# Kernel optimization log

Hardware: AMD Instinct MI355X
Metric: run time of the kernel (lower is better)

Reference implementation:

```python
import jax, jax.numpy as jnp
import numpy as np

B, S, D, E = 4, 2048, 512, 32

def setup_inputs() -> dict:
    key = jax.random.key(0)
    k1, k2, k3 = jax.random.split(key, 3)
    x = jax.random.normal(k1, (B, S, D), dtype=jnp.float32)
    # glorot-ish scaling for weights
    gate_w = jax.random.normal(k2, (D, E), dtype=jnp.float32) * (1.0 / np.sqrt(D))
    gate_b = jnp.zeros((E,), dtype=jnp.float32)
    expert_w = jax.random.normal(k3, (E, D, D), dtype=jnp.float32) * (1.0 / np.sqrt(D))
    return {"x": x, "gate_w": gate_w, "gate_b": gate_b, "expert_w": expert_w}

def reference(x, gate_w, gate_b, expert_w):
    # gate_scores: [B,S,E] (context=None -> route on x itself)
    gate = jax.nn.softmax(jnp.einsum('bsd,de->bse', x, gate_w) + gate_b, axis=-1)
    # Dense soft-MoE: sum_e gate[b,s,e] * (x[b,s,:] @ expert_w[e])
    # Single einsum avoids materializing the [B,S,E,D] intermediate.
    out = jnp.einsum('bse,bsd,edf->bsf', gate, x, expert_w)
    return out
```

## Files before the change

kernel.cpp:

```cpp
#include <hip/hip_runtime.h>

#define TOK 8192
#define DIM 512
#define NE  32
#define KTOT (NE * DIM)

#define BM 128
#define BN 128
#define BK 64

typedef float f32x4 __attribute__((ext_vector_type(4)));
typedef short s16x8 __attribute__((ext_vector_type(8)));

typedef const void __attribute__((address_space(1)))* gp1_t;
typedef void __attribute__((address_space(3)))* lp3_t;

__device__ __forceinline__ void gl_lds16(const void* g, void* l) {
    __builtin_amdgcn_global_load_lds((gp1_t)g, (lp3_t)l, 16, 0, 0);
}

__device__ __forceinline__ ushort f2bf(float f) {
    unsigned u = __builtin_bit_cast(unsigned, f);
    unsigned r = (u + 0x7fffu + ((u >> 16) & 1u)) >> 16;
    return (ushort)r;
}

__global__ __launch_bounds__(256) void k_cvt_wt(const float* __restrict__ w,
                                                ushort* __restrict__ wt) {
    __shared__ float tile[32][33];
    const int e = blockIdx.z;
    const int f0 = blockIdx.x * 32;
    const int d0 = blockIdx.y * 32;
    const int tx = threadIdx.x, ty = threadIdx.y;
    const float* we = w + (size_t)e * DIM * DIM;
#pragma unroll
    for (int i = ty; i < 32; i += 8)
        tile[i][tx] = we[(size_t)(d0 + i) * DIM + f0 + tx];
    __syncthreads();
#pragma unroll
    for (int i = ty; i < 32; i += 8)
        wt[(size_t)(f0 + i) * KTOT + e * DIM + d0 + tx] = f2bf(tile[tx][i]);
}

__global__ __launch_bounds__(256) void k_gates(const float* __restrict__ x,
                                               const float* __restrict__ gw,
                                               const float* __restrict__ gb,
                                               float* __restrict__ G,
                                               ushort* __restrict__ xb) {
    __shared__ float xs[DIM];
    __shared__ float part[256];
    __shared__ float logits[NE];
    const int t = blockIdx.x;
    const int tid = threadIdx.x;
    float v0 = x[(size_t)t * DIM + tid];
    float v1 = x[(size_t)t * DIM + tid + 256];
    xs[tid] = v0;
    xs[tid + 256] = v1;
    xb[(size_t)t * DIM + tid] = f2bf(v0);
    xb[(size_t)t * DIM + tid + 256] = f2bf(v1);
    __syncthreads();
    const int e = tid & 31;
    const int ch = tid >> 5;
    float s = 0.f;
#pragma unroll 8
    for (int i = 0; i < 64; ++i) {
        int d = ch * 64 + i;
        s += xs[d] * gw[d * NE + e];
    }
    part[tid] = s;
    __syncthreads();
    if (tid < NE) {
        float l = gb[tid];
#pragma unroll
        for (int c = 0; c < 8; ++c) l += part[c * 32 + tid];
        logits[tid] = l;
    }
    __syncthreads();
    float ex = 0.f;
    if (tid < NE) {
        float mx = -1e30f;
#pragma unroll
        for (int o = 0; o < NE; ++o) mx = fmaxf(mx, logits[o]);
        ex = expf(logits[tid] - mx);
        part[tid] = ex;
    }
    __syncthreads();
    if (tid < NE) {
        float sum = 0.f;
#pragma unroll
        for (int o = 0; o < NE; ++o) sum += part[o];
        G[(size_t)t * NE + tid] = ex / sum;
    }
}

__global__ __launch_bounds__(512, 2) void k_moe_gemm(const ushort* __restrict__ xb,
                                                     const ushort* __restrict__ wt,
                                                     const float* __restrict__ G,
                                                     float* __restrict__ out0,
                                                     float* __restrict__ out1) {
    __shared__ __align__(16) ushort As[BM * BK];
    __shared__ __align__(16) ushort Bs[BN * BK];
    __shared__ float Gs[BM][17];

    const int tid = threadIdx.x;
    const int m0 = blockIdx.y * BM;
    const int n0 = blockIdx.x * BN;
    const int e0 = blockIdx.z * 16;
    float* __restrict__ dst = blockIdx.z ? out1 : out0;

    for (int i = tid; i < BM * 16; i += 512) {
        int r = i >> 4, c = i & 15;
        Gs[r][c] = G[(size_t)(m0 + r) * NE + e0 + c];
    }

    const int lane = tid & 63;
    const int wave = tid >> 6;
    const int wm = (wave & 3) * 32;
    const int wn = (wave >> 2) * 64;
    const int l15 = lane & 15;
    const int q = lane >> 4;
    const int keyR = l15 & 7;

    const f32x4 zv = {0.f, 0.f, 0.f, 0.f};
    f32x4 acc[2][4];
#pragma unroll
    for (int i = 0; i < 2; ++i)
#pragma unroll
        for (int j = 0; j < 4; ++j) acc[i][j] = zv;

    const int srow = tid >> 3;
    const int chunk = tid & 7;
    const int scol = ((chunk ^ (srow & 7)) * 8);
    const ushort* aBase = xb + (size_t)(m0 + srow) * DIM + scol;
    const ushort* bBase = wt + (size_t)(n0 + srow) * KTOT + scol;
    char* aLds = (char*)As + tid * 16;
    char* bLds = (char*)Bs + tid * 16;

#pragma unroll 1
    for (int ee = 0; ee < 16; ++ee) {
        const int e = e0 + ee;
        f32x4 pacc[2][4];
#pragma unroll
        for (int i = 0; i < 2; ++i)
#pragma unroll
            for (int j = 0; j < 4; ++j) pacc[i][j] = zv;

#pragma unroll 1
        for (int kt = 0; kt < 8; ++kt) {
            const int kd = kt * BK;
            const ushort* aS = aBase + kd;
            const ushort* bS = bBase + (size_t)e * DIM + kd;
            gl_lds16(aS, aLds);
            gl_lds16(aS + (size_t)64 * DIM, aLds + 8192);
            gl_lds16(bS, bLds);
            gl_lds16(bS + (size_t)64 * KTOT, bLds + 8192);
            __syncthreads();
#pragma unroll
            for (int ks = 0; ks < 2; ++ks) {
                const int swz = ((ks * 4 + q) ^ keyR) * 16;
                s16x8 a[2], b[4];
#pragma unroll
                for (int i = 0; i < 2; ++i)
                    a[i] = *(const s16x8*)((const char*)As +
                           (wm + i * 16 + l15) * (BK * 2) + swz);
#pragma unroll
                for (int j = 0; j < 4; ++j)
                    b[j] = *(const s16x8*)((const char*)Bs +
                           (wn + j * 16 + l15) * (BK * 2) + swz);
#pragma unroll
                for (int i = 0; i < 2; ++i)
#pragma unroll
                    for (int j = 0; j < 4; ++j)
                        pacc[i][j] = __builtin_amdgcn_mfma_f32_16x16x32_bf16(
                            a[i], b[j], pacc[i][j], 0, 0, 0);
            }
            __syncthreads();
        }

#pragma unroll
        for (int i = 0; i < 2; ++i) {
            const int tl = wm + i * 16 + q * 4;
            const float g0 = Gs[tl + 0][ee];
            const float g1 = Gs[tl + 1][ee];
            const float g2 = Gs[tl + 2][ee];
            const float g3 = Gs[tl + 3][ee];
#pragma unroll
            for (int j = 0; j < 4; ++j) {
                acc[i][j][0] += g0 * pacc[i][j][0];
                acc[i][j][1] += g1 * pacc[i][j][1];
                acc[i][j][2] += g2 * pacc[i][j][2];
                acc[i][j][3] += g3 * pacc[i][j][3];
            }
        }
    }

#pragma unroll
    for (int i = 0; i < 2; ++i) {
        const int tl = m0 + wm + i * 16 + q * 4;
#pragma unroll
        for (int j = 0; j < 4; ++j) {
            const int f = n0 + wn + j * 16 + l15;
            float* p = dst + (size_t)tl * DIM + f;
            p[0 * DIM] = acc[i][j][0];
            p[1 * DIM] = acc[i][j][1];
            p[2 * DIM] = acc[i][j][2];
            p[3 * DIM] = acc[i][j][3];
        }
    }
}

__global__ __launch_bounds__(256) void k_reduce(float* __restrict__ out,
                                                const float* __restrict__ P) {
    int i = (blockIdx.x * 256 + threadIdx.x) * 4;
    float4 a = *(const float4*)(out + i);
    float4 b = *(const float4*)(P + i);
    a.x += b.x; a.y += b.y; a.z += b.z; a.w += b.w;
    *(float4*)(out + i) = a;
}

extern "C" void kernel_launch(void* const* d_in, const int* in_sizes, int n_in,
                              void* d_out, int out_size, void* d_ws, size_t ws_size,
                              hipStream_t stream) {
    const float* x  = (const float*)d_in[0];
    const float* gw = (const float*)d_in[1];
    const float* gb = (const float*)d_in[2];
    const float* w  = (const float*)d_in[3];
    float* out = (float*)d_out;

    char* ws = (char*)d_ws;
    ushort* xb = (ushort*)ws;
    ushort* wt = (ushort*)(ws + (8u << 20));
    float*  G  = (float*)(ws + (24u << 20));
    float*  P  = (float*)(ws + (25u << 20));

    k_cvt_wt<<<dim3(16, 16, NE), dim3(32, 8, 1), 0, stream>>>(w, wt);
    k_gates<<<dim3(TOK), dim3(256), 0, stream>>>(x, gw, gb, G, xb);
    k_moe_gemm<<<dim3(DIM / BN, TOK / BM, 2), dim3(512), 0, stream>>>(xb, wt, G, out, P);
    k_reduce<<<dim3(TOK * DIM / (256 * 4)), dim3(256), 0, stream>>>(out, P);
}
```

Baseline: 257.8 us.

## Double-buffer GEMM tiles with expert-inner loop and fuse prep kernels

The GEMM main loop is reordered so the k-tile is outer and the expert is inner. The A tile is reused across all 16 experts, and the A/B tiles are double-buffered so the next global-to-LDS load is issued before the current tile's MFMAs run, which removes one barrier per step. The weight transpose/convert and gating kernels are merged into one launch, and the gating now handles 8 tokens per block with shuffle-based softmax. Gate values are stored transposed for vector reads. The cost is double the LDS per block, which may limit occupancy at 2 blocks per CU.

```diff
diff --git a/kernel.cpp b/kernel.cpp
--- a/kernel.cpp
+++ b/kernel.cpp
@@ -25,71 +25,59 @@
     return (ushort)r;
 }
 
-__global__ __launch_bounds__(256) void k_cvt_wt(const float* __restrict__ w,
-                                                ushort* __restrict__ wt) {
-    __shared__ float tile[32][33];
-    const int e = blockIdx.z;
-    const int f0 = blockIdx.x * 32;
-    const int d0 = blockIdx.y * 32;
-    const int tx = threadIdx.x, ty = threadIdx.y;
-    const float* we = w + (size_t)e * DIM * DIM;
-#pragma unroll
-    for (int i = ty; i < 32; i += 8)
-        tile[i][tx] = we[(size_t)(d0 + i) * DIM + f0 + tx];
-    __syncthreads();
-#pragma unroll
-    for (int i = ty; i < 32; i += 8)
-        wt[(size_t)(f0 + i) * KTOT + e * DIM + d0 + tx] = f2bf(tile[tx][i]);
-}
-
-__global__ __launch_bounds__(256) void k_gates(const float* __restrict__ x,
-                                               const float* __restrict__ gw,
-                                               const float* __restrict__ gb,
-                                               float* __restrict__ G,
-                                               ushort* __restrict__ xb) {
-    __shared__ float xs[DIM];
-    __shared__ float part[256];
-    __shared__ float logits[NE];
-    const int t = blockIdx.x;
+__global__ __launch_bounds__(256) void k_prep(const float* __restrict__ w,
+                                              ushort* __restrict__ wt,
+                                              const float* __restrict__ x,
+                                              const float* __restrict__ gw,
+                                              const float* __restrict__ gb,
+                                              float* __restrict__ G,
+                                              ushort* __restrict__ xb) {
+    __shared__ __align__(16) char smem[64 * 65 * 4];
+    const int bx = blockIdx.x;
     const int tid = threadIdx.x;
-    float v0 = x[(size_t)t * DIM + tid];
-    float v1 = x[(size_t)t * DIM + tid + 256];
-    xs[tid] = v0;
-    xs[tid + 256] = v1;
-    xb[(size_t)t * DIM + tid] = f2bf(v0);
-    xb[(size_t)t * DIM + tid + 256] = f2bf(v1);
-    __syncthreads();
-    const int e = tid & 31;
-    const int ch = tid >> 5;
-    float s = 0.f;
+    if (bx < 2048) {
+        float (*tile)[65] = (float(*)[65])smem;
+        const int e = bx >> 6;
+        const int f0 = ((bx >> 3) & 7) * 64;
+        const int d0 = (bx & 7) * 64;
+        const int tx = tid & 63, ty = tid >> 6;
+        const float* we = w + (size_t)e * DIM * DIM;
+#pragma unroll
+        for (int i = ty; i < 64; i += 4)
+            tile[i][tx] = we[(size_t)(d0 + i) * DIM + f0 + tx];
+        __syncthreads();
+#pragma unroll
+        for (int i = ty; i < 64; i += 4)
+            wt[(size_t)(f0 + i) * KTOT + e * DIM + d0 + tx] = f2bf(tile[tx][i]);
+    } else {
+        float* xs = (float*)smem;
+        const int t0 = (bx - 2048) * 8;
+        const float* xBase = x + (size_t)t0 * DIM;
+#pragma unroll
+        for (int k = 0; k < 4; ++k) {
+            int i4 = (k * 256 + tid) * 4;
+            float4 v = *(const float4*)(xBase + i4);
+            xs[i4 + 0] = v.x; xs[i4 + 1] = v.y; xs[i4 + 2] = v.z; xs[i4 + 3] = v.w;
+            ushort4 o;
+            o.x = f2bf(v.x); o.y = f2bf(v.y); o.z = f2bf(v.z); o.w = f2bf(v.w);
+            *(ushort4*)(xb + (size_t)t0 * DIM + i4) = o;
+        }
+        __syncthreads();
+        const int tok = tid >> 5;
+        const int e = tid & 31;
+        float l = gb[e];
+        const float* xr = xs + tok * DIM;
 #pragma unroll 8
-    for (int i = 0; i < 64; ++i) {
-        int d = ch * 64 + i;
-        s += xs[d] * gw[d * NE + e];
-    }
-    part[tid] = s;
-    __syncthreads();
-    if (tid < NE) {
-        float l = gb[tid];
-#pragma unroll
-        for (int c = 0; c < 8; ++c) l += part[c * 32 + tid];
-        logits[tid] = l;
-    }
-    __syncthreads();
-    float ex = 0.f;
-    if (tid < NE) {
-        float mx = -1e30f;
-#pragma unroll
-        for (int o = 0; o < NE; ++o) mx = fmaxf(mx, logits[o]);
-        ex = expf(logits[tid] - mx);
-        part[tid] = ex;
-    }
-    __syncthreads();
-    if (tid < NE) {
-        float sum = 0.f;
-#pragma unroll
-        for (int o = 0; o < NE; ++o) sum += part[o];
-        G[(size_t)t * NE + tid] = ex / sum;
+        for (int d = 0; d < DIM; ++d)
+            l += xr[d] * gw[d * NE + e];
+        float mx = l;
+#pragma unroll
+        for (int m = 16; m >= 1; m >>= 1) mx = fmaxf(mx, __shfl_xor(mx, m));
+        float ex = expf(l - mx);
+        float s = ex;
+#pragma unroll
+        for (int m = 16; m >= 1; m >>= 1) s += __shfl_xor(s, m);
+        G[(size_t)(t0 + tok) * NE + e] = ex / s;
     }
 }
 
@@ -98,9 +86,9 @@
                                                      const float* __restrict__ G,
                                                      float* __restrict__ out0,
                                                      float* __restrict__ out1) {
-    __shared__ __align__(16) ushort As[BM * BK];
-    __shared__ __align__(16) ushort Bs[BN * BK];
-    __shared__ float Gs[BM][17];
+    __shared__ __align__(16) ushort As[2][BM * BK];
+    __shared__ __align__(16) ushort Bs[2][BN * BK];
+    __shared__ float Gs[16][BM];
 
     const int tid = threadIdx.x;
     const int m0 = blockIdx.y * BM;
@@ -108,9 +96,9 @@
     const int e0 = blockIdx.z * 16;
     float* __restrict__ dst = blockIdx.z ? out1 : out0;
 
-    for (int i = tid; i < BM * 16; i += 512) {
-        int r = i >> 4, c = i & 15;
-        Gs[r][c] = G[(size_t)(m0 + r) * NE + e0 + c];
+    for (int i = tid; i < 16 * BM; i += 512) {
+        int e = i >> 7, r = i & 127;
+        Gs[e][r] = G[(size_t)(m0 + r) * NE + e0 + e];
     }
 
     const int lane = tid & 63;
@@ -121,76 +109,98 @@
     const int q = lane >> 4;
     const int keyR = l15 & 7;
 
-    const f32x4 zv = {0.f, 0.f, 0.f, 0.f};
-    f32x4 acc[2][4];
-#pragma unroll
-    for (int i = 0; i < 2; ++i)
-#pragma unroll
-        for (int j = 0; j < 4; ++j) acc[i][j] = zv;
+    const int swz0 = ((q) ^ keyR) * 16;
+    const int swz1 = ((4 + q) ^ keyR) * 16;
+    const int rowA0 = (wm + l15) * 128;
+    const int rowA1 = (wm + 16 + l15) * 128;
+    const int rowB0 = (wn + l15) * 128;
+    const int rowB1 = (wn + 16 + l15) * 128;
+    const int rowB2 = (wn + 32 + l15) * 128;
+    const int rowB3 = (wn + 48 + l15) * 128;
 
     const int srow = tid >> 3;
     const int chunk = tid & 7;
     const int scol = ((chunk ^ (srow & 7)) * 8);
     const ushort* aBase = xb + (size_t)(m0 + srow) * DIM + scol;
-    const ushort* bBase = wt + (size_t)(n0 + srow) * KTOT + scol;
-    char* aLds = (char*)As + tid * 16;
-    char* bLds = (char*)Bs + tid * 16;
+    const ushort* bBase = wt + (size_t)(n0 + srow) * KTOT + (size_t)e0 * DIM + scol;
+    const int ldsOff = tid * 16;
+
+    const f32x4 zv = {0.f, 0.f, 0.f, 0.f};
+    f32x4 acc[2][4];
+#pragma unroll
+    for (int i = 0; i < 2; ++i)
+#pragma unroll
+        for (int j = 0; j < 4; ++j) acc[i][j] = zv;
+
+    gl_lds16(aBase, (char*)As[0] + ldsOff);
+    gl_lds16(aBase + (size_t)64 * DIM, (char*)As[0] + 8192 + ldsOff);
+    gl_lds16(bBase, (char*)Bs[0] + ldsOff);
+    gl_lds16(bBase + (size_t)64 * KTOT, (char*)Bs[0] + 8192 + ldsOff);
+    __syncthreads();
 
 #pragma unroll 1
-    for (int ee = 0; ee < 16; ++ee) {
-        const int e = e0 + ee;
-        f32x4 pacc[2][4];
-#pragma unroll
-        for (int i = 0; i < 2; ++i)
-#pragma unroll
-            for (int j = 0; j < 4; ++j) pacc[i][j] = zv;
-
+    for (int kt = 0; kt < 8; ++kt) {
+        const char* Ab = (const char*)As[kt & 1];
 #pragma unroll 1
-        for (int kt = 0; kt < 8; ++kt) {
-            const int kd = kt * BK;
-            const ushort* aS = aBase + kd;
-            const ushort* bS = bBase + (size_t)e * DIM + kd;
-            gl_lds16(aS, aLds);
-            gl_lds16(aS + (size_t)64 * DIM, aLds + 8192);
-            gl_lds16(bS, bLds);
-            gl_lds16(bS + (size_t)64 * KTOT, bLds + 8192);
-            __syncthreads();
+        for (int ee = 0; ee < 16; ++ee) {
+            const int gn = kt * 16 + ee + 1;
+            if (gn < 128) {
+                const ushort* bN = bBase + (size_t)(gn & 15) * DIM + (gn >> 4) * BK;
+                char* bL = (char*)Bs[gn & 1] + ldsOff;
+                gl_lds16(bN, bL);
+                gl_lds16(bN + (size_t)64 * KTOT, bL + 8192);
+                if (ee == 15) {
+                    const ushort* aN = aBase + (kt + 1) * BK;
+                    char* aL = (char*)As[(kt + 1) & 1] + ldsOff;
+                    gl_lds16(aN, aL);
+                    gl_lds16(aN + (size_t)64 * DIM, aL + 8192);
+                }
+            }
+
+            const char* Bb = (const char*)Bs[ee & 1];
+            f32x4 pacc[2][4];
 #pragma unroll
             for (int ks = 0; ks < 2; ++ks) {
-                const int swz = ((ks * 4 + q) ^ keyR) * 16;
-                s16x8 a[2], b[4];
-#pragma unroll
-                for (int i = 0; i < 2; ++i)
-                    a[i] = *(const s16x8*)((const char*)As +
-                           (wm + i * 16 + l15) * (BK * 2) + swz);
-#pragma unroll
-                for (int j = 0; j < 4; ++j)
-                    b[j] = *(const s16x8*)((const char*)Bs +
-                           (wn + j * 16 + l15) * (BK * 2) + swz);
-#pragma unroll
-                for (int i = 0; i < 2; ++i)
-#pragma unroll
-                    for (int j = 0; j < 4; ++j)
-                        pacc[i][j] = __builtin_amdgcn_mfma_f32_16x16x32_bf16(
-                            a[i], b[j], pacc[i][j], 0, 0, 0);
+                const int swz = ks ? swz1 : swz0;
+                s16x8 a0 = *(const s16x8*)(Ab + rowA0 + swz);
+                s16x8 a1 = *(const s16x8*)(Ab + rowA1 + swz);
+                s16x8 b0 = *(const s16x8*)(Bb + rowB0 + swz);
+                s16x8 b1 = *(const s16x8*)(Bb + rowB1 + swz);
+                s16x8 b2 = *(const s16x8*)(Bb + rowB2 + swz);
+                s16x8 b3 = *(const s16x8*)(Bb + rowB3 + swz);
+                if (ks == 0) {
+                    pacc[0][0] = __builtin_amdgcn_mfma_f32_16x16x32_bf16(a0, b0, zv, 0, 0, 0);
+                    pacc[0][1] = __builtin_amdgcn_mfma_f32_16x16x32_bf16(a0, b1, zv, 0, 0, 0);
+                    pacc[0][2] = __builtin_amdgcn_mfma_f32_16x16x32_bf16(a0, b2, zv, 0, 0, 0);
+                    pacc[0][3] = __builtin_amdgcn_mfma_f32_16x16x32_bf16(a0, b3, zv, 0, 0, 0);
+                    pacc[1][0] = __builtin_amdgcn_mfma_f32_16x16x32_bf16(a1, b0, zv, 0, 0, 0);
+                    pacc[1][1] = __builtin_amdgcn_mfma_f32_16x16x32_bf16(a1, b1, zv, 0, 0, 0);
+                    pacc[1][2] = __builtin_amdgcn_mfma_f32_16x16x32_bf16(a1, b2, zv, 0, 0, 0);
+                    pacc[1][3] = __builtin_amdgcn_mfma_f32_16x16x32_bf16(a1, b3, zv, 0, 0, 0);
+                } else {
+                    pacc[0][0] = __builtin_amdgcn_mfma_f32_16x16x32_bf16(a0, b0, pacc[0][0], 0, 0, 0);
+                    pacc[0][1] = __builtin_amdgcn_mfma_f32_16x16x32_bf16(a0, b1, pacc[0][1], 0, 0, 0);
+                    pacc[0][2] = __builtin_amdgcn_mfma_f32_16x16x32_bf16(a0, b2, pacc[0][2], 0, 0, 0);
+                    pacc[0][3] = __builtin_amdgcn_mfma_f32_16x16x32_bf16(a0, b3, pacc[0][3], 0, 0, 0);
+                    pacc[1][0] = __builtin_amdgcn_mfma_f32_16x16x32_bf16(a1, b0, pacc[1][0], 0, 0, 0);
+                    pacc[1][1] = __builtin_amdgcn_mfma_f32_16x16x32_bf16(a1, b1, pacc[1][1], 0, 0, 0);
+                    pacc[1][2] = __builtin_amdgcn_mfma_f32_16x16x32_bf16(a1, b2, pacc[1][2], 0, 0, 0);
+                    pacc[1][3] = __builtin_amdgcn_mfma_f32_16x16x32_bf16(a1, b3, pacc[1][3], 0, 0, 0);
+                }
+            }
+
+#pragma unroll
+            for (int i = 0; i < 2; ++i) {
+                const f32x4 gt = *(const f32x4*)&Gs[ee][wm + i * 16 + q * 4];
+#pragma unroll
+                for (int j = 0; j < 4; ++j) {
+                    acc[i][j][0] += gt[0] * pacc[i][j][0];
+                    acc[i][j][1] += gt[1] * pacc[i][j][1];
+                    acc[i][j][2] += gt[2] * pacc[i][j][2];
+                    acc[i][j][3] += gt[3] * pacc[i][j][3];
+                }
             }
             __syncthreads();
-        }
-
-#pragma unroll
-        for (int i = 0; i < 2; ++i) {
-            const int tl = wm + i * 16 + q * 4;
-            const float g0 = Gs[tl + 0][ee];
-            const float g1 = Gs[tl + 1][ee];
-            const float g2 = Gs[tl + 2][ee];
-            const float g3 = Gs[tl + 3][ee];
-#pragma unroll
-            for (int j = 0; j < 4; ++j) {
-                acc[i][j][0] += g0 * pacc[i][j][0];
-                acc[i][j][1] += g1 * pacc[i][j][1];
-                acc[i][j][2] += g2 * pacc[i][j][2];
-                acc[i][j][3] += g3 * pacc[i][j][3];
-            }
         }
     }
 
@@ -233,8 +243,7 @@
     float*  G  = (float*)(ws + (24u << 20));
     float*  P  = (float*)(ws + (25u << 20));
 
-    k_cvt_wt<<<dim3(16, 16, NE), dim3(32, 8, 1), 0, stream>>>(w, wt);
-    k_gates<<<dim3(TOK), dim3(256), 0, stream>>>(x, gw, gb, G, xb);
+    k_prep<<<dim3(2048 + TOK / 8), dim3(256), 0, stream>>>(w, wt, x, gw, gb, G, xb);
     k_moe_gemm<<<dim3(DIM / BN, TOK / BM, 2), dim3(512), 0, stream>>>(xb, wt, G, out, P);
-    k_reduce<<<dim3(TOK * DIM / (256 * 4)), dim3(256), 0, stream>>>(out, P);
-}
+    k_reduce<<<dim3(TOK * DIM / 1024), dim3(256), 0, stream>>>(out, P);
+}
```

New measurement: 255.7 us. Within noise of the previous version (-0.8%).
